# Kernel tuning notes

Hardware: AMD Instinct MI355X
Metric: run time of the kernel (lower is better)

The kernel has to match this reference:

```python
import jax, jax.numpy as jnp
import numpy as np

B, C, H, W = 8, 512, 64, 64
KD, OD = 64, 512

def setup_inputs() -> dict:
    key = jax.random.key(0)
    ks = jax.random.split(key, 8)
    s = 0.05
    return {
        "x":     jax.random.normal(ks[0], (B, C, H, W), dtype=jnp.float32),
        "q_w":   jax.random.normal(ks[1], (KD, C), dtype=jnp.float32) * s,
        "q_b":   jax.random.normal(ks[2], (KD,), dtype=jnp.float32) * s,
        "k_w":   jax.random.normal(ks[3], (KD, C), dtype=jnp.float32) * s,
        "k_b":   jax.random.normal(ks[4], (KD,), dtype=jnp.float32) * s,
        "v_w":   jax.random.normal(ks[5], (OD, C), dtype=jnp.float32) * s,
        "v_b":   jax.random.normal(ks[6], (OD,), dtype=jnp.float32) * s,
        "gamma": jax.random.normal(ks[7], (1,), dtype=jnp.float32) * s,
    }

def reference(x, q_w, q_b, k_w, k_b, v_w, v_b, gamma):
    b, c, h, w = x.shape
    n = h * w
    xf = x.reshape(b, c, n)                                   # [B, C, N]
    # 1x1 convs == per-position matmuls
    q = jnp.einsum('kc,bcn->bkn', q_w, xf) + q_b[:, None]     # [B, KD, N]
    k = jnp.einsum('kc,bcn->bkn', k_w, xf) + k_b[:, None]     # [B, KD, N]
    v = jnp.einsum('oc,bcn->bon', v_w, xf) + v_b[:, None]     # [B, OD, N]
    # energy[b, i, j] = <q[:, i], k[:, j]>  (query permuted to [B, N, KD])
    energy = jnp.einsum('bki,bkj->bij', q, k)                 # [B, N, N]
    attn = jax.nn.softmax(energy, axis=-1)                    # softmax over j
    # out = V @ attn^T : out[b, o, i] = sum_j v[b, o, j] * attn[b, i, j]
    out = jnp.einsum('boj,bij->boi', v, attn)                 # [B, OD, N]
    out = gamma[0] * out + v
    return out.reshape(b, -1, h, w)
```

## Files before the change

### kernel.cpp

```cpp
#include <hip/hip_runtime.h>
#include <hip/hip_bf16.h>

#define BATCH 8
#define CDIM  512
#define NPOS  4096
#define KDQK  64
#define ODIM  512

typedef __attribute__((ext_vector_type(8)))  short short8v;
typedef __attribute__((ext_vector_type(16))) float f32x16;

static __device__ __forceinline__ unsigned short f2bf(float f) {
    union { __hip_bfloat16 h; unsigned short u; } cv;
    cv.h = __float2bfloat16(f);
    return cv.u;
}
static __device__ __forceinline__ float bf2f(unsigned short u) {
    union { unsigned short u; __hip_bfloat16 h; } cv;
    cv.u = u;
    return __bfloat162float(cv.h);
}

static __device__ __forceinline__ void gload_lds16(const unsigned short* g, unsigned short* s) {
    __builtin_amdgcn_global_load_lds((const __attribute__((address_space(1))) unsigned int*)g,
                                     (__attribute__((address_space(3))) unsigned int*)s, 16, 0, 0);
}

static __device__ __forceinline__ int cvtpk(float a, float b) {
    int r;
    asm("v_cvt_pk_bf16_f32 %0, %1, %2" : "=v"(r) : "v"(a), "v"(b));
    return r;
}

#if __has_builtin(__builtin_amdgcn_exp2f)
static __device__ __forceinline__ float exp2_raw(float x) { return __builtin_amdgcn_exp2f(x); }
#else
static __device__ __forceinline__ float exp2_raw(float x) { return exp2f(x); }
#endif

__global__ __launch_bounds__(256) void wconv_kernel(const float* __restrict__ qw,
                                                    const float* __restrict__ kw,
                                                    const float* __restrict__ vw,
                                                    unsigned short* __restrict__ wq,
                                                    unsigned short* __restrict__ wk,
                                                    unsigned short* __restrict__ wv) {
    int idx = blockIdx.x * 256 + threadIdx.x;
    if (idx < 32768)        wq[idx]          = f2bf(qw[idx]);
    else if (idx < 65536)   wk[idx - 32768]  = f2bf(kw[idx - 32768]);
    else if (idx < 327680)  wv[idx - 65536]  = f2bf(vw[idx - 65536]);
}

__global__ __launch_bounds__(256) void xpose_kernel(const float* __restrict__ x,
                                                    unsigned short* __restrict__ xT) {
    __shared__ float xs[64][65];
    const int b = blockIdx.z, c0 = blockIdx.y * 64, n0 = blockIdx.x * 64;
    const int t = threadIdx.x;
    #pragma unroll
    for (int it = 0; it < 4; ++it) {
        int lin = it * 256 + t;
        int c = lin >> 4, nq = lin & 15;
        const float4 v = *reinterpret_cast<const float4*>(
            x + ((size_t)(b * CDIM + c0 + c) * NPOS + n0 + nq * 4));
        xs[c][nq * 4 + 0] = v.x; xs[c][nq * 4 + 1] = v.y;
        xs[c][nq * 4 + 2] = v.z; xs[c][nq * 4 + 3] = v.w;
    }
    __syncthreads();
    #pragma unroll
    for (int it = 0; it < 4; ++it) {
        int lin = it * 256 + t;
        int n = lin >> 4, cq = lin & 15;
        ushort4 u;
        u.x = f2bf(xs[cq * 4 + 0][n]); u.y = f2bf(xs[cq * 4 + 1][n]);
        u.z = f2bf(xs[cq * 4 + 2][n]); u.w = f2bf(xs[cq * 4 + 3][n]);
        *reinterpret_cast<ushort4*>(xT + ((size_t)(b * NPOS + n0 + n) * CDIM + c0 + cq * 4)) = u;
    }
}

template <int TRANS>
__global__ __launch_bounds__(256) void proj_kernel(const unsigned short* __restrict__ W,
                                                   const float* __restrict__ bias,
                                                   const unsigned short* __restrict__ xT,
                                                   unsigned short* __restrict__ Y,
                                                   float scale) {
    __shared__ unsigned short Wl[64][64];
    __shared__ unsigned short Xl[64][64];
    const int b = blockIdx.z, r0 = blockIdx.y * 64, n0 = blockIdx.x * 64;
    const int t = threadIdx.x, wave = t >> 6, lane = t & 63, hi = lane >> 5, lo = lane & 31;
    const int wr = wave >> 1, wc = wave & 1;

    f32x16 acc;
    #pragma unroll
    for (int q = 0; q < 16; ++q) acc[q] = 0.f;

    for (int ck = 0; ck < CDIM; ck += 64) {
        __syncthreads();
        #pragma unroll
        for (int it = 0; it < 2; ++it) {
            int lin = it * 256 + t;
            int r = lin >> 3, c8 = lin & 7;
            int4 v = *reinterpret_cast<const int4*>(W + ((size_t)(r0 + r) * CDIM + ck + c8 * 8));
            *reinterpret_cast<int4*>(&Wl[r][(c8 ^ (r & 7)) * 8]) = v;
        }
        #pragma unroll
        for (int it = 0; it < 2; ++it) {
            int lin = it * 256 + t;
            int n = lin >> 3, c8 = lin & 7;
            int4 v = *reinterpret_cast<const int4*>(
                xT + ((size_t)(b * NPOS + n0 + n) * CDIM + ck + c8 * 8));
            *reinterpret_cast<int4*>(&Xl[n][(c8 ^ (n & 7)) * 8]) = v;
        }
        __syncthreads();
        const int ar = wr * 32 + lo, bn = wc * 32 + lo;
        #pragma unroll
        for (int ks = 0; ks < 4; ++ks) {
            int chunk = 2 * ks + hi;
            short8v a  = *reinterpret_cast<const short8v*>(&Wl[ar][(chunk ^ (ar & 7)) * 8]);
            short8v bb = *reinterpret_cast<const short8v*>(&Xl[bn][(chunk ^ (bn & 7)) * 8]);
            acc = __builtin_amdgcn_mfma_f32_32x32x16_bf16(a, bb, acc, 0, 0, 0);
        }
    }

    const int n = n0 + wc * 32 + lo;
    if (TRANS) {
        #pragma unroll
        for (int g = 0; g < 4; ++g) {
            int rbase = wr * 32 + g * 8 + hi * 4;
            ushort4 u;
            u.x = f2bf((acc[4 * g + 0] + bias[r0 + rbase + 0]) * scale);
            u.y = f2bf((acc[4 * g + 1] + bias[r0 + rbase + 1]) * scale);
            u.z = f2bf((acc[4 * g + 2] + bias[r0 + rbase + 2]) * scale);
            u.w = f2bf((acc[4 * g + 3] + bias[r0 + rbase + 3]) * scale);
            *reinterpret_cast<ushort4*>(Y + ((size_t)(b * NPOS + n) * KDQK + r0 + rbase)) = u;
        }
    } else {
        #pragma unroll
        for (int q = 0; q < 16; ++q) {
            int r = r0 + wr * 32 + (q & 3) + 8 * (q >> 2) + 4 * hi;
            Y[(size_t)(b * ODIM + r) * NPOS + n] = f2bf((acc[q] + bias[r]) * scale);
        }
    }
}

__global__ __launch_bounds__(512, 2) void attn_kernel(const unsigned short* __restrict__ Qt,
                                                      const unsigned short* __restrict__ Kt,
                                                      const unsigned short* __restrict__ V,
                                                      const float* __restrict__ gamma_p,
                                                      float* __restrict__ out) {
    __shared__ __align__(16) unsigned short Kbuf[2][64 * 64];
    __shared__ __align__(16) unsigned short Vbuf[2][256 * 64];
    __shared__ __align__(16) unsigned short Pl[256 * 64];
    __shared__ float cb[256];
    __shared__ float lb[256];

    const int bid = blockIdx.x;
    const int b = bid & 7, r = bid >> 3, odh = r & 1, qt = r >> 1;
    const int i0 = qt * 256, od0 = odh * 256;
    const int tid = threadIdx.x, w = tid >> 6, l = tid & 63, lo = l & 31, hi = l >> 5;
    const int key = lo & 7;

    const int krow = w * 8 + (l >> 3);
    const unsigned short* kp = Kt + ((size_t)b * NPOS + krow) * 64 + (((l & 7) ^ (krow & 7)) << 3);
    const unsigned short* vp[4];
    int vrow_[4];
    #pragma unroll
    for (int v = 0; v < 4; ++v) {
        int vrow = w * 32 + v * 8 + (l >> 3);
        vrow_[v] = vrow;
        vp[v] = V + ((size_t)(b * ODIM + od0 + vrow)) * NPOS + (((l & 7) ^ (vrow & 7)) << 3);
    }

    short8v qf[4];
    {
        const unsigned short* qb = Qt + ((size_t)b * NPOS + i0 + w * 32 + lo) * 64 + hi * 8;
        #pragma unroll
        for (int kc = 0; kc < 4; ++kc)
            qf[kc] = *reinterpret_cast<const short8v*>(qb + kc * 16);
    }

    f32x16 acc[8];
    #pragma unroll
    for (int it = 0; it < 8; ++it)
        #pragma unroll
        for (int q = 0; q < 16; ++q) acc[it][q] = 0.f;

    float m_run = -1e30f, l_run = 0.f;

    gload_lds16(kp, &Kbuf[0][w * 512]);
    #pragma unroll
    for (int v = 0; v < 4; ++v) gload_lds16(vp[v], &Vbuf[0][(w * 32 + v * 8) * 64]);
    __syncthreads();

    for (int t = 0; t < NPOS / 64; ++t) {
        const int cur = t & 1;

        f32x16 s0, s1;
        #pragma unroll
        for (int q = 0; q < 16; ++q) { s0[q] = 0.f; s1[q] = 0.f; }
        const unsigned short* KB = &Kbuf[cur][0];
        #pragma unroll
        for (int kc = 0; kc < 4; ++kc) {
            int cpos = ((2 * kc + hi) ^ key) << 3;
            short8v a0 = *reinterpret_cast<const short8v*>(KB + lo * 64 + cpos);
            short8v a1 = *reinterpret_cast<const short8v*>(KB + (32 + lo) * 64 + cpos);
            s0 = __builtin_amdgcn_mfma_f32_32x32x16_bf16(a0, qf[kc], s0, 0, 0, 0);
            s1 = __builtin_amdgcn_mfma_f32_32x32x16_bf16(a1, qf[kc], s1, 0, 0, 0);
        }
        float mx = fmaxf(s0[0], s1[0]);
        #pragma unroll
        for (int q = 1; q < 16; ++q) mx = fmaxf(mx, fmaxf(s0[q], s1[q]));
        mx = fmaxf(mx, __shfl_xor(mx, 32));

        bool g = mx > m_run + 12.f;
        float c = g ? exp2_raw(m_run - mx) : 1.f;
        if (g) m_run = mx;

        float rs = 0.f;
        #pragma unroll
        for (int q = 0; q < 16; ++q) {
            s0[q] = exp2_raw(s0[q] - m_run); rs += s0[q];
            s1[q] = exp2_raw(s1[q] - m_run); rs += s1[q];
        }
        rs += __shfl_xor(rs, 32);
        l_run = l_run * c + rs;
        if (hi == 0) cb[w * 32 + lo] = c;

        {
            unsigned short* prow = &Pl[(w * 32 + lo) * 64];
            #pragma unroll
            for (int m = 0; m < 4; ++m) {
                int w0 = cvtpk(s0[4 * m + 0], s0[4 * m + 1]);
                int w1 = cvtpk(s0[4 * m + 2], s0[4 * m + 3]);
                *reinterpret_cast<int2*>(prow + ((m ^ key) << 3) + hi * 4) = make_int2(w0, w1);
                int w2 = cvtpk(s1[4 * m + 0], s1[4 * m + 1]);
                int w3 = cvtpk(s1[4 * m + 2], s1[4 * m + 3]);
                *reinterpret_cast<int2*>(prow + (((4 + m) ^ key) << 3) + hi * 4) = make_int2(w2, w3);
            }
        }
        __syncthreads();

        if (t + 1 < NPOS / 64) {
            const int nb = cur ^ 1;
            gload_lds16(kp + (size_t)(t + 1) * 64 * 64, &Kbuf[nb][w * 512]);
            #pragma unroll
            for (int v = 0; v < 4; ++v)
                gload_lds16(vp[v] + (t + 1) * 64, &Vbuf[nb][(w * 32 + v * 8) * 64]);
        }

        float cv[8];
        #pragma unroll
        for (int it = 0; it < 8; ++it) cv[it] = cb[it * 32 + lo];
        bool need = false;
        #pragma unroll
        for (int it = 0; it < 8; ++it) need = need || (cv[it] != 1.f);
        if (__any(need)) {
            #pragma unroll
            for (int it = 0; it < 8; ++it)
                #pragma unroll
                for (int q = 0; q < 16; ++q) acc[it][q] *= cv[it];
        }

        const unsigned short* VB = &Vbuf[cur][0];
        short8v va[4];
        #pragma unroll
        for (int kc = 0; kc < 4; ++kc)
            va[kc] = *reinterpret_cast<const short8v*>(
                VB + (w * 32 + lo) * 64 + (((2 * kc + hi) ^ key) << 3));

        #pragma unroll
        for (int it = 0; it < 8; ++it) {
            const unsigned short* prow = &Pl[(it * 32 + lo) * 64];
            #pragma unroll
            for (int kc = 0; kc < 4; ++kc) {
                short8v pb = *reinterpret_cast<const short8v*>(
                    prow + (((2 * kc + hi) ^ key) << 3));
                acc[it] = __builtin_amdgcn_mfma_f32_32x32x16_bf16(va[kc], pb, acc[it], 0, 0, 0);
            }
        }
        __syncthreads();
    }

    if (hi == 0) lb[w * 32 + lo] = l_run;
    __syncthreads();
    float linv[8];
    #pragma unroll
    for (int it = 0; it < 8; ++it) linv[it] = 1.0f / lb[it * 32 + lo];
    const float gm = gamma_p[0];
    #pragma unroll
    for (int it = 0; it < 8; ++it) {
        #pragma unroll
        for (int q = 0; q < 16; ++q) {
            int od = od0 + w * 32 + (q & 3) + 8 * (q >> 2) + 4 * hi;
            int i = i0 + it * 32 + lo;
            size_t addr = ((size_t)b * ODIM + od) * NPOS + i;
            out[addr] = gm * acc[it][q] * linv[it] + bf2f(V[addr]);
        }
    }
}

extern "C" void kernel_launch(void* const* d_in, const int* in_sizes, int n_in,
                              void* d_out, int out_size, void* d_ws, size_t ws_size,
                              hipStream_t stream) {
    const float* x     = (const float*)d_in[0];
    const float* qw    = (const float*)d_in[1];
    const float* qb    = (const float*)d_in[2];
    const float* kw    = (const float*)d_in[3];
    const float* kb    = (const float*)d_in[4];
    const float* vw    = (const float*)d_in[5];
    const float* vb    = (const float*)d_in[6];
    const float* gamma = (const float*)d_in[7];
    float* out = (float*)d_out;

    char* ws = (char*)d_ws;
    unsigned short* xT = (unsigned short*)(ws);
    unsigned short* wq = (unsigned short*)(ws + 33554432);
    unsigned short* wk = (unsigned short*)(ws + 33619968);
    unsigned short* wv = (unsigned short*)(ws + 33685504);
    unsigned short* Qt = (unsigned short*)(ws + 34209792);
    unsigned short* Kt = (unsigned short*)(ws + 38404096);
    unsigned short* Vn = (unsigned short*)(ws + 42598400);

    wconv_kernel<<<1280, 256, 0, stream>>>(qw, kw, vw, wq, wk, wv);
    xpose_kernel<<<dim3(64, 8, 8), 256, 0, stream>>>(x, xT);
    proj_kernel<1><<<dim3(64, 1, 8), 256, 0, stream>>>(wq, qb, xT, Qt, 1.44269504f);
    proj_kernel<1><<<dim3(64, 1, 8), 256, 0, stream>>>(wk, kb, xT, Kt, 1.0f);
    proj_kernel<0><<<dim3(64, 8, 8), 256, 0, stream>>>(wv, vb, xT, Vn, 1.0f);
    attn_kernel<<<256, 512, 0, stream>>>(Qt, Kt, Vn, gamma, out);
}
```

Measured before the change: 373.4 us.

## Retile projection to 128x128 double-buffered GEMM and shrink attention tiles

Replaces the 64x64 projection kernel with a 128x128-tile kernel that double-buffers W and X through direct global-to-LDS loads. It fuses the Q and K projections into one launch by stacking their weights, assuming wq and wk sit next to each other in the workspace. The attention kernel moves from 512-thread blocks over 256 queries with 64-key steps to 256-thread blocks over 128 queries with 32-key steps, giving 512 blocks and a smaller LDS footprint. In exchange there are twice as many loop iterations and barriers per key, and less reuse of each V tile.

```diff
diff --git a/kernel.cpp b/kernel.cpp
--- a/kernel.cpp
+++ b/kernel.cpp
@@ -76,138 +76,174 @@
     }
 }
 
-template <int TRANS>
-__global__ __launch_bounds__(256) void proj_kernel(const unsigned short* __restrict__ W,
-                                                   const float* __restrict__ bias,
-                                                   const unsigned short* __restrict__ xT,
-                                                   unsigned short* __restrict__ Y,
-                                                   float scale) {
-    __shared__ unsigned short Wl[64][64];
-    __shared__ unsigned short Xl[64][64];
-    const int b = blockIdx.z, r0 = blockIdx.y * 64, n0 = blockIdx.x * 64;
-    const int t = threadIdx.x, wave = t >> 6, lane = t & 63, hi = lane >> 5, lo = lane & 31;
-    const int wr = wave >> 1, wc = wave & 1;
-
-    f32x16 acc;
-    #pragma unroll
-    for (int q = 0; q < 16; ++q) acc[q] = 0.f;
-
-    for (int ck = 0; ck < CDIM; ck += 64) {
+template <int MODE>
+__global__ __launch_bounds__(256, 2) void proj128_kernel(const unsigned short* __restrict__ W,
+                                                         const float* __restrict__ bq,
+                                                         const float* __restrict__ bk,
+                                                         const unsigned short* __restrict__ xT,
+                                                         unsigned short* __restrict__ Ya,
+                                                         unsigned short* __restrict__ Yb) {
+    __shared__ __align__(16) unsigned short Wl[2][128 * 64];
+    __shared__ __align__(16) unsigned short Xl[2][128 * 64];
+    const int b = blockIdx.z, r0 = blockIdx.y * 128, n0 = blockIdx.x * 128;
+    const int tid = threadIdx.x, w = tid >> 6, l = tid & 63, lo = l & 31, hi = l >> 5;
+    const int wr = w >> 1, wc = w & 1;
+
+    const unsigned short* wsrc[4];
+    const unsigned short* xsrc[4];
+    #pragma unroll
+    for (int g = 0; g < 4; ++g) {
+        int row = g * 32 + w * 8 + (l >> 3);
+        int ch = ((l & 7) ^ (row & 7)) << 3;
+        wsrc[g] = W + (size_t)(r0 + row) * CDIM + ch;
+        xsrc[g] = xT + ((size_t)(b * NPOS + n0 + row)) * CDIM + ch;
+    }
+
+    f32x16 acc[2][2];
+    #pragma unroll
+    for (int a = 0; a < 2; ++a)
+        #pragma unroll
+        for (int q = 0; q < 16; ++q) { acc[a][0][q] = 0.f; acc[a][1][q] = 0.f; }
+
+    #pragma unroll
+    for (int g = 0; g < 4; ++g) {
+        gload_lds16(wsrc[g], &Wl[0][(g * 32 + w * 8) * 64]);
+        gload_lds16(xsrc[g], &Xl[0][(g * 32 + w * 8) * 64]);
+    }
+    __syncthreads();
+
+    for (int t = 0; t < 8; ++t) {
+        const int cur = t & 1;
+        if (t < 7) {
+            #pragma unroll
+            for (int g = 0; g < 4; ++g) {
+                gload_lds16(wsrc[g] + (t + 1) * 64, &Wl[cur ^ 1][(g * 32 + w * 8) * 64]);
+                gload_lds16(xsrc[g] + (t + 1) * 64, &Xl[cur ^ 1][(g * 32 + w * 8) * 64]);
+            }
+        }
+        #pragma unroll
+        for (int kc = 0; kc < 4; ++kc) {
+            const int cpos = ((2 * kc + hi) ^ (lo & 7)) << 3;
+            short8v wa0 = *reinterpret_cast<const short8v*>(&Wl[cur][(wr * 64 + lo) * 64 + cpos]);
+            short8v wa1 = *reinterpret_cast<const short8v*>(&Wl[cur][(wr * 64 + 32 + lo) * 64 + cpos]);
+            short8v xb0 = *reinterpret_cast<const short8v*>(&Xl[cur][(wc * 64 + lo) * 64 + cpos]);
+            short8v xb1 = *reinterpret_cast<const short8v*>(&Xl[cur][(wc * 64 + 32 + lo) * 64 + cpos]);
+            acc[0][0] = __builtin_amdgcn_mfma_f32_32x32x16_bf16(wa0, xb0, acc[0][0], 0, 0, 0);
+            acc[0][1] = __builtin_amdgcn_mfma_f32_32x32x16_bf16(wa0, xb1, acc[0][1], 0, 0, 0);
+            acc[1][0] = __builtin_amdgcn_mfma_f32_32x32x16_bf16(wa1, xb0, acc[1][0], 0, 0, 0);
+            acc[1][1] = __builtin_amdgcn_mfma_f32_32x32x16_bf16(wa1, xb1, acc[1][1], 0, 0, 0);
+        }
         __syncthreads();
-        #pragma unroll
-        for (int it = 0; it < 2; ++it) {
-            int lin = it * 256 + t;
-            int r = lin >> 3, c8 = lin & 7;
-            int4 v = *reinterpret_cast<const int4*>(W + ((size_t)(r0 + r) * CDIM + ck + c8 * 8));
-            *reinterpret_cast<int4*>(&Wl[r][(c8 ^ (r & 7)) * 8]) = v;
-        }
-        #pragma unroll
-        for (int it = 0; it < 2; ++it) {
-            int lin = it * 256 + t;
-            int n = lin >> 3, c8 = lin & 7;
-            int4 v = *reinterpret_cast<const int4*>(
-                xT + ((size_t)(b * NPOS + n0 + n) * CDIM + ck + c8 * 8));
-            *reinterpret_cast<int4*>(&Xl[n][(c8 ^ (n & 7)) * 8]) = v;
-        }
-        __syncthreads();
-        const int ar = wr * 32 + lo, bn = wc * 32 + lo;
-        #pragma unroll
-        for (int ks = 0; ks < 4; ++ks) {
-            int chunk = 2 * ks + hi;
-            short8v a  = *reinterpret_cast<const short8v*>(&Wl[ar][(chunk ^ (ar & 7)) * 8]);
-            short8v bb = *reinterpret_cast<const short8v*>(&Xl[bn][(chunk ^ (bn & 7)) * 8]);
-            acc = __builtin_amdgcn_mfma_f32_32x32x16_bf16(a, bb, acc, 0, 0, 0);
-        }
-    }
-
-    const int n = n0 + wc * 32 + lo;
-    if (TRANS) {
-        #pragma unroll
-        for (int g = 0; g < 4; ++g) {
-            int rbase = wr * 32 + g * 8 + hi * 4;
-            ushort4 u;
-            u.x = f2bf((acc[4 * g + 0] + bias[r0 + rbase + 0]) * scale);
-            u.y = f2bf((acc[4 * g + 1] + bias[r0 + rbase + 1]) * scale);
-            u.z = f2bf((acc[4 * g + 2] + bias[r0 + rbase + 2]) * scale);
-            u.w = f2bf((acc[4 * g + 3] + bias[r0 + rbase + 3]) * scale);
-            *reinterpret_cast<ushort4*>(Y + ((size_t)(b * NPOS + n) * KDQK + r0 + rbase)) = u;
+    }
+
+    if (MODE == 1) {
+        const float scale = wr ? 1.0f : 1.44269504f;
+        const float* bias = wr ? bk : bq;
+        unsigned short* Y = wr ? Yb : Ya;
+        #pragma unroll
+        for (int a = 0; a < 2; ++a) {
+            #pragma unroll
+            for (int c = 0; c < 2; ++c) {
+                const int n = n0 + wc * 64 + c * 32 + lo;
+                #pragma unroll
+                for (int g = 0; g < 4; ++g) {
+                    int rb = a * 32 + g * 8 + hi * 4;
+                    float4 b4 = *reinterpret_cast<const float4*>(bias + rb);
+                    ushort4 u;
+                    u.x = f2bf((acc[a][c][4 * g + 0] + b4.x) * scale);
+                    u.y = f2bf((acc[a][c][4 * g + 1] + b4.y) * scale);
+                    u.z = f2bf((acc[a][c][4 * g + 2] + b4.z) * scale);
+                    u.w = f2bf((acc[a][c][4 * g + 3] + b4.w) * scale);
+                    *reinterpret_cast<ushort4*>(Y + ((size_t)(b * NPOS + n) * KDQK + rb)) = u;
+                }
+            }
         }
     } else {
         #pragma unroll
-        for (int q = 0; q < 16; ++q) {
-            int r = r0 + wr * 32 + (q & 3) + 8 * (q >> 2) + 4 * hi;
-            Y[(size_t)(b * ODIM + r) * NPOS + n] = f2bf((acc[q] + bias[r]) * scale);
-        }
-    }
-}
-
-__global__ __launch_bounds__(512, 2) void attn_kernel(const unsigned short* __restrict__ Qt,
+        for (int a = 0; a < 2; ++a) {
+            #pragma unroll
+            for (int c = 0; c < 2; ++c) {
+                const int n = n0 + wc * 64 + c * 32 + lo;
+                #pragma unroll
+                for (int g = 0; g < 4; ++g) {
+                    int rb = r0 + wr * 64 + a * 32 + g * 8 + hi * 4;
+                    float4 b4 = *reinterpret_cast<const float4*>(bq + rb);
+                    Ya[(size_t)(b * ODIM + rb + 0) * NPOS + n] = f2bf(acc[a][c][4 * g + 0] + b4.x);
+                    Ya[(size_t)(b * ODIM + rb + 1) * NPOS + n] = f2bf(acc[a][c][4 * g + 1] + b4.y);
+                    Ya[(size_t)(b * ODIM + rb + 2) * NPOS + n] = f2bf(acc[a][c][4 * g + 2] + b4.z);
+                    Ya[(size_t)(b * ODIM + rb + 3) * NPOS + n] = f2bf(acc[a][c][4 * g + 3] + b4.w);
+                }
+            }
+        }
+    }
+}
+
+__global__ __launch_bounds__(256, 2) void attn_kernel(const unsigned short* __restrict__ Qt,
                                                       const unsigned short* __restrict__ Kt,
                                                       const unsigned short* __restrict__ V,
                                                       const float* __restrict__ gamma_p,
                                                       float* __restrict__ out) {
-    __shared__ __align__(16) unsigned short Kbuf[2][64 * 64];
-    __shared__ __align__(16) unsigned short Vbuf[2][256 * 64];
-    __shared__ __align__(16) unsigned short Pl[256 * 64];
-    __shared__ float cb[256];
-    __shared__ float lb[256];
+    __shared__ __align__(16) unsigned short Kbuf[2][32 * 64];
+    __shared__ __align__(16) unsigned short Vbuf[2][256 * 32];
+    __shared__ __align__(16) unsigned short Pl[128 * 32];
+    __shared__ float cb[128];
+    __shared__ float lb[128];
 
     const int bid = blockIdx.x;
     const int b = bid & 7, r = bid >> 3, odh = r & 1, qt = r >> 1;
-    const int i0 = qt * 256, od0 = odh * 256;
+    const int i0 = qt * 128, od0 = odh * 256;
     const int tid = threadIdx.x, w = tid >> 6, l = tid & 63, lo = l & 31, hi = l >> 5;
-    const int key = lo & 7;
+    const int pvw = w >> 1, ow = w & 1;
+    const int keyr = (lo >> 1) & 3;
 
     const int krow = w * 8 + (l >> 3);
-    const unsigned short* kp = Kt + ((size_t)b * NPOS + krow) * 64 + (((l & 7) ^ (krow & 7)) << 3);
+    const unsigned short* kp = Kt + ((size_t)b * NPOS + krow) * KDQK + (((l & 7) ^ (krow & 7)) << 3);
     const unsigned short* vp[4];
-    int vrow_[4];
     #pragma unroll
     for (int v = 0; v < 4; ++v) {
-        int vrow = w * 32 + v * 8 + (l >> 3);
-        vrow_[v] = vrow;
-        vp[v] = V + ((size_t)(b * ODIM + od0 + vrow)) * NPOS + (((l & 7) ^ (vrow & 7)) << 3);
+        int vrow = v * 64 + w * 16 + (l >> 2);
+        vp[v] = V + ((size_t)(b * ODIM + od0 + vrow)) * NPOS + (((l & 3) ^ ((vrow >> 1) & 3)) << 3);
     }
 
     short8v qf[4];
     {
-        const unsigned short* qb = Qt + ((size_t)b * NPOS + i0 + w * 32 + lo) * 64 + hi * 8;
+        const unsigned short* qb = Qt + ((size_t)b * NPOS + i0 + w * 32 + lo) * KDQK + hi * 8;
         #pragma unroll
         for (int kc = 0; kc < 4; ++kc)
             qf[kc] = *reinterpret_cast<const short8v*>(qb + kc * 16);
     }
 
-    f32x16 acc[8];
-    #pragma unroll
-    for (int it = 0; it < 8; ++it)
-        #pragma unroll
-        for (int q = 0; q < 16; ++q) acc[it][q] = 0.f;
+    f32x16 acc[2][4];
+    #pragma unroll
+    for (int it = 0; it < 2; ++it)
+        #pragma unroll
+        for (int odg = 0; odg < 4; ++odg)
+            #pragma unroll
+            for (int q = 0; q < 16; ++q) acc[it][odg][q] = 0.f;
 
     float m_run = -1e30f, l_run = 0.f;
 
     gload_lds16(kp, &Kbuf[0][w * 512]);
     #pragma unroll
-    for (int v = 0; v < 4; ++v) gload_lds16(vp[v], &Vbuf[0][(w * 32 + v * 8) * 64]);
+    for (int v = 0; v < 4; ++v) gload_lds16(vp[v], &Vbuf[0][(v * 64 + w * 16) * 32]);
     __syncthreads();
 
-    for (int t = 0; t < NPOS / 64; ++t) {
+    for (int t = 0; t < NPOS / 32; ++t) {
         const int cur = t & 1;
 
-        f32x16 s0, s1;
-        #pragma unroll
-        for (int q = 0; q < 16; ++q) { s0[q] = 0.f; s1[q] = 0.f; }
+        f32x16 s;
+        #pragma unroll
+        for (int q = 0; q < 16; ++q) s[q] = 0.f;
         const unsigned short* KB = &Kbuf[cur][0];
         #pragma unroll
         for (int kc = 0; kc < 4; ++kc) {
-            int cpos = ((2 * kc + hi) ^ key) << 3;
-            short8v a0 = *reinterpret_cast<const short8v*>(KB + lo * 64 + cpos);
-            short8v a1 = *reinterpret_cast<const short8v*>(KB + (32 + lo) * 64 + cpos);
-            s0 = __builtin_amdgcn_mfma_f32_32x32x16_bf16(a0, qf[kc], s0, 0, 0, 0);
-            s1 = __builtin_amdgcn_mfma_f32_32x32x16_bf16(a1, qf[kc], s1, 0, 0, 0);
-        }
-        float mx = fmaxf(s0[0], s1[0]);
-        #pragma unroll
-        for (int q = 1; q < 16; ++q) mx = fmaxf(mx, fmaxf(s0[q], s1[q]));
+            short8v a = *reinterpret_cast<const short8v*>(
+                KB + lo * 64 + (((2 * kc + hi) ^ (lo & 7)) << 3));
+            s = __builtin_amdgcn_mfma_f32_32x32x16_bf16(a, qf[kc], s, 0, 0, 0);
+        }
+        float mx = s[0];
+        #pragma unroll
+        for (int q = 1; q < 16; ++q) mx = fmaxf(mx, s[q]);
         mx = fmaxf(mx, __shfl_xor(mx, 32));
 
         bool g = mx > m_run + 12.f;
@@ -216,64 +252,51 @@
 
         float rs = 0.f;
         #pragma unroll
-        for (int q = 0; q < 16; ++q) {
-            s0[q] = exp2_raw(s0[q] - m_run); rs += s0[q];
-            s1[q] = exp2_raw(s1[q] - m_run); rs += s1[q];
-        }
+        for (int q = 0; q < 16; ++q) { s[q] = exp2_raw(s[q] - m_run); rs += s[q]; }
         rs += __shfl_xor(rs, 32);
         l_run = l_run * c + rs;
         if (hi == 0) cb[w * 32 + lo] = c;
 
         {
-            unsigned short* prow = &Pl[(w * 32 + lo) * 64];
+            unsigned short* prow = &Pl[(w * 32 + lo) * 32];
             #pragma unroll
             for (int m = 0; m < 4; ++m) {
-                int w0 = cvtpk(s0[4 * m + 0], s0[4 * m + 1]);
-                int w1 = cvtpk(s0[4 * m + 2], s0[4 * m + 3]);
-                *reinterpret_cast<int2*>(prow + ((m ^ key) << 3) + hi * 4) = make_int2(w0, w1);
-                int w2 = cvtpk(s1[4 * m + 0], s1[4 * m + 1]);
-                int w3 = cvtpk(s1[4 * m + 2], s1[4 * m + 3]);
-                *reinterpret_cast<int2*>(prow + (((4 + m) ^ key) << 3) + hi * 4) = make_int2(w2, w3);
+                int w0 = cvtpk(s[4 * m + 0], s[4 * m + 1]);
+                int w1 = cvtpk(s[4 * m + 2], s[4 * m + 3]);
+                *reinterpret_cast<int2*>(prow + ((m ^ keyr) << 3) + hi * 4) = make_int2(w0, w1);
             }
         }
         __syncthreads();
 
-        if (t + 1 < NPOS / 64) {
+        if (t + 1 < NPOS / 32) {
             const int nb = cur ^ 1;
-            gload_lds16(kp + (size_t)(t + 1) * 64 * 64, &Kbuf[nb][w * 512]);
+            gload_lds16(kp + (size_t)(t + 1) * 2048, &Kbuf[nb][w * 512]);
             #pragma unroll
             for (int v = 0; v < 4; ++v)
-                gload_lds16(vp[v] + (t + 1) * 64, &Vbuf[nb][(w * 32 + v * 8) * 64]);
-        }
-
-        float cv[8];
-        #pragma unroll
-        for (int it = 0; it < 8; ++it) cv[it] = cb[it * 32 + lo];
-        bool need = false;
-        #pragma unroll
-        for (int it = 0; it < 8; ++it) need = need || (cv[it] != 1.f);
-        if (__any(need)) {
-            #pragma unroll
-            for (int it = 0; it < 8; ++it)
+                gload_lds16(vp[v] + (t + 1) * 32, &Vbuf[nb][(v * 64 + w * 16) * 32]);
+        }
+
+        float cv0 = cb[pvw * 64 + lo];
+        float cv1 = cb[pvw * 64 + 32 + lo];
+        if (__any(cv0 != 1.f || cv1 != 1.f)) {
+            #pragma unroll
+            for (int odg = 0; odg < 4; ++odg)
                 #pragma unroll
-                for (int q = 0; q < 16; ++q) acc[it][q] *= cv[it];
+                for (int q = 0; q < 16; ++q) { acc[0][odg][q] *= cv0; acc[1][odg][q] *= cv1; }
         }
 
         const unsigned short* VB = &Vbuf[cur][0];
-        short8v va[4];
-        #pragma unroll
-        for (int kc = 0; kc < 4; ++kc)
-            va[kc] = *reinterpret_cast<const short8v*>(
-                VB + (w * 32 + lo) * 64 + (((2 * kc + hi) ^ key) << 3));
-
-        #pragma unroll
-        for (int it = 0; it < 8; ++it) {
-            const unsigned short* prow = &Pl[(it * 32 + lo) * 64];
-            #pragma unroll
-            for (int kc = 0; kc < 4; ++kc) {
-                short8v pb = *reinterpret_cast<const short8v*>(
-                    prow + (((2 * kc + hi) ^ key) << 3));
-                acc[it] = __builtin_amdgcn_mfma_f32_32x32x16_bf16(va[kc], pb, acc[it], 0, 0, 0);
+        #pragma unroll
+        for (int kc = 0; kc < 2; ++kc) {
+            const int cpos = (((2 * kc + hi) ^ keyr) << 3);
+            short8v pb0 = *reinterpret_cast<const short8v*>(&Pl[(pvw * 64 + lo) * 32] + cpos);
+            short8v pb1 = *reinterpret_cast<const short8v*>(&Pl[(pvw * 64 + 32 + lo) * 32] + cpos);
+            #pragma unroll
+            for (int odg = 0; odg < 4; ++odg) {
+                short8v va = *reinterpret_cast<const short8v*>(
+                    VB + (ow * 128 + odg * 32 + lo) * 32 + cpos);
+                acc[0][odg] = __builtin_amdgcn_mfma_f32_32x32x16_bf16(va, pb0, acc[0][odg], 0, 0, 0);
+                acc[1][odg] = __builtin_amdgcn_mfma_f32_32x32x16_bf16(va, pb1, acc[1][odg], 0, 0, 0);
             }
         }
         __syncthreads();
@@ -281,18 +304,21 @@
 
     if (hi == 0) lb[w * 32 + lo] = l_run;
     __syncthreads();
-    float linv[8];
-    #pragma unroll
-    for (int it = 0; it < 8; ++it) linv[it] = 1.0f / lb[it * 32 + lo];
+    float linv0 = 1.0f / lb[pvw * 64 + lo];
+    float linv1 = 1.0f / lb[pvw * 64 + 32 + lo];
     const float gm = gamma_p[0];
     #pragma unroll
-    for (int it = 0; it < 8; ++it) {
-        #pragma unroll
-        for (int q = 0; q < 16; ++q) {
-            int od = od0 + w * 32 + (q & 3) + 8 * (q >> 2) + 4 * hi;
-            int i = i0 + it * 32 + lo;
-            size_t addr = ((size_t)b * ODIM + od) * NPOS + i;
-            out[addr] = gm * acc[it][q] * linv[it] + bf2f(V[addr]);
+    for (int it = 0; it < 2; ++it) {
+        float linv = it ? linv1 : linv0;
+        #pragma unroll
+        for (int odg = 0; odg < 4; ++odg) {
+            #pragma unroll
+            for (int q = 0; q < 16; ++q) {
+                int od = od0 + ow * 128 + odg * 32 + (q & 3) + 8 * (q >> 2) + 4 * hi;
+                int i = i0 + pvw * 64 + it * 32 + lo;
+                size_t addr = ((size_t)b * ODIM + od) * NPOS + i;
+                out[addr] = gm * acc[it][odg][q] * linv + bf2f(V[addr]);
+            }
         }
     }
 }
@@ -321,8 +347,7 @@
 
     wconv_kernel<<<1280, 256, 0, stream>>>(qw, kw, vw, wq, wk, wv);
     xpose_kernel<<<dim3(64, 8, 8), 256, 0, stream>>>(x, xT);
-    proj_kernel<1><<<dim3(64, 1, 8), 256, 0, stream>>>(wq, qb, xT, Qt, 1.44269504f);
-    proj_kernel<1><<<dim3(64, 1, 8), 256, 0, stream>>>(wk, kb, xT, Kt, 1.0f);
-    proj_kernel<0><<<dim3(64, 8, 8), 256, 0, stream>>>(wv, vb, xT, Vn, 1.0f);
-    attn_kernel<<<256, 512, 0, stream>>>(Qt, Kt, Vn, gamma, out);
-}
+    proj128_kernel<1><<<dim3(32, 1, 8), 256, 0, stream>>>(wq, qb, kb, xT, Qt, Kt);
+    proj128_kernel<0><<<dim3(32, 4, 8), 256, 0, stream>>>(wv, vb, vb, xT, Vn, Vn);
+    attn_kernel<<<512, 256, 0, stream>>>(Qt, Kt, Vn, gamma, out);
+}
```

Result: slower. 403.4 us (+8.0%).
